# Performance work log

Measured on AMD Instinct MI355X. Metric: run time of the kernel, lower is better.

The kernel has to match this reference:

```python
import jax, jax.numpy as jnp
import numpy as np

N_AGENTS = 8; N_DUMMY = 16; BATCH = 1024; PLAN = 128; HID = 256

def setup_inputs():
    key = jax.random.key(0)
    ks = jax.random.split(key, 12)
    N, ND, B, P, H = N_AGENTS, N_DUMMY, BATCH, PLAN, HID
    plans = jax.random.normal(ks[0], (B, N, P), jnp.float32)
    keep = jax.random.bernoulli(ks[1], 0.7, (B, N))  # ragged communication pattern
    comm_plans = jax.random.normal(ks[2], (B, N, P), jnp.float32) * keep[:, :, None]
    coord_hiddens = 0.1 * jax.random.normal(ks[3], (N, 2, B, H), jnp.float32)
    dummy_noise = jax.random.normal(ks[4], (N, ND - N, B, 2 * P), jnp.float32)
    s = 0.05
    Wi_f = s * jax.random.normal(ks[5], (N, 3 * H, 2 * P), jnp.float32)
    Wh_f = s * jax.random.normal(ks[6], (N, 3 * H, H), jnp.float32)
    Wi_b = s * jax.random.normal(ks[7], (N, 3 * H, 2 * P), jnp.float32)
    Wh_b = s * jax.random.normal(ks[8], (N, 3 * H, H), jnp.float32)
    ln_g = jnp.ones((N, 2 * H), jnp.float32)
    ln_b = jnp.zeros((N, 2 * H), jnp.float32)
    W1 = s * jax.random.normal(ks[9], (N, H, 2 * H), jnp.float32)
    b1 = jnp.zeros((N, H), jnp.float32)
    W2 = s * jax.random.normal(ks[10], (N, 2, H), jnp.float32)
    b2 = jnp.zeros((N, 2), jnp.float32)
    return dict(plans=plans, comm_plans=comm_plans, coord_hiddens=coord_hiddens,
                dummy_noise=dummy_noise, Wi_f=Wi_f, Wh_f=Wh_f, Wi_b=Wi_b, Wh_b=Wh_b,
                ln_g=ln_g, ln_b=ln_b, W1=W1, b1=b1, W2=W2, b2=b2)

def _gru_scan(xs, h0, Wi, Wh, valid):
    # PyTorch GRU cell (biases are zero-initialized in RecurrentHead), length-masked
    H = h0.shape[-1]
    gi_all = jnp.einsum('tbi,gi->tbg', xs, Wi)  # (T,B,3H) input projections, one GEMM
    def step(h, inp):
        gi, v = inp
        gh = h @ Wh.T
        r = jax.nn.sigmoid(gi[:, :H] + gh[:, :H])
        z = jax.nn.sigmoid(gi[:, H:2 * H] + gh[:, H:2 * H])
        n = jnp.tanh(gi[:, 2 * H:] + r * gh[:, 2 * H:])
        hn = (1.0 - z) * n + z * h
        h = jnp.where(v[:, None], hn, h)            # packed: no update past seq end
        return h, jnp.where(v[:, None], hn, 0.0)    # pad_packed returns zeros there
    hT, out = jax.lax.scan(step, h0, (gi_all, valid))
    return out, hT

def _forward(plans, comm_plans, coord_hiddens, dummy_noise, Wi_f, Wh_f, Wi_b, Wh_b, ln_g, ln_b, W1, b1, W2, b2):
    B, N, P = plans.shape
    ND = N_DUMMY
    # comm_plans[~any(any(comm_plans))] = plans[...]
    empty = ~jnp.any(jnp.any(comm_plans != 0, -1), -1)            # (B,)
    comm = jnp.where(empty[:, None, None], plans, comm_plans)     # (B,N,P)
    mask_real = jnp.any(comm != 0, -1).T                          # (N,B)
    mask = jnp.concatenate([mask_real, jnp.ones((ND - N, B), bool)], 0)  # (ND,B)
    mask_flat = mask.reshape(-1)
    seq_len = mask.sum(0)                                         # (B,)
    t_idx = jnp.arange(ND)[:, None]
    packed_mask = t_idx < seq_len[None, :]                        # (ND,B)
    pm_flat = packed_mask.reshape(-1)
    # torch boolean-index / masked_scatter consume elements in flat row-major order;
    # we reproduce those exact semantics.
    src_idx = jnp.nonzero(mask_flat, size=ND * B, fill_value=0)[0]
    rank_pack = jnp.cumsum(pm_flat) - 1
    cum_scat = jnp.cumsum(mask_flat) - 1
    rev_idx = jnp.where(packed_mask, seq_len[None, :] - 1 - t_idx, 0)

    def pack(x):  # compact_seq[packed_mask] = x[batch_mask]
        xf = x.reshape(ND * B, -1)
        return jnp.where(pm_flat[:, None], xf[src_idx[rank_pack]], 0.0).reshape(ND, B, -1)

    def scatter(s):  # zeros.masked_scatter(mask, scores)
        st, sb = cum_scat // B, cum_scat % B
        return jnp.where(mask_flat[:, None], s[st, sb], 0.0).reshape(ND, B, -1)

    def rev(a):  # per-column reversal within valid length (for bidirectional GRU)
        g = jnp.take_along_axis(a, jnp.broadcast_to(rev_idx[:, :, None], a.shape), axis=0)
        return jnp.where(packed_mask[:, :, None], g, 0.0)

    plans_t = plans.transpose(1, 0, 2)  # (N,B,P): plans[:, i] per agent

    def per_agent(plan_i, dn_i, hxs_i, wif, whf, wib, whb, g, bta, w1, bb1, w2, bb2):
        others = jnp.concatenate([jnp.broadcast_to(plan_i[:, None, :], comm.shape), comm], -1)  # (B,N,2P)
        x = jnp.concatenate([others.transpose(1, 0, 2), dn_i], 0)  # (ND,B,2P) with randn dummy rows
        cseq = pack(x)
        out_f, hf = _gru_scan(cseq, hxs_i[0], wif, whf, packed_mask)
        out_b_r, hb = _gru_scan(rev(cseq), hxs_i[1], wib, whb, packed_mask)
        out_b = rev(out_b_r)
        scores = scatter(jnp.concatenate([out_f, out_b], -1))  # (ND,B,2H)
        mu = scores.mean(-1, keepdims=True)
        var = ((scores - mu) ** 2).mean(-1, keepdims=True)
        scores = (scores - mu) * jax.lax.rsqrt(var + 1e-5) * g + bta  # LayerNorm
        h1 = jax.nn.relu(jnp.einsum('tbc,hc->tbh', scores, w1) + bb1)
        cm = jnp.einsum('tbh,oh->tbo', h1, w2) + bb2               # (ND,B,2)
        return cm, jnp.stack([hf, hb])                              # (2,B,H)

    coord_masks, coord_rnn_hxs = jax.vmap(per_agent)(
        plans_t, dummy_noise, coord_hiddens, Wi_f, Wh_f, Wi_b, Wh_b, ln_g, ln_b, W1, b1, W2, b2)
    return coord_masks, coord_rnn_hxs

def reference(plans, comm_plans, coord_hiddens, dummy_noise, Wi_f, Wh_f, Wi_b, Wh_b, ln_g, ln_b, W1, b1, W2, b2):
    return _forward(plans, comm_plans, coord_hiddens, dummy_noise, Wi_f, Wh_f, Wi_b, Wh_b, ln_g, ln_b, W1, b1, W2, b2)
```

## Files before the change

### kernel.cpp

```cpp
#include <hip/hip_runtime.h>


typedef _Float16 f16;
typedef __attribute__((ext_vector_type(4))) _Float16 f16x4;
typedef __attribute__((ext_vector_type(8))) _Float16 f16x8;
typedef __attribute__((ext_vector_type(4))) float floatx4;

__device__ __forceinline__ float sigf(float x) { return 1.0f / (1.0f + __expf(-x)); }
__device__ __forceinline__ float tanhfast(float x) {
    float e = __expf(2.0f * x);
    return 1.0f - 2.0f / (e + 1.0f);
}

__device__ __forceinline__ void gl16(const f16* g, f16* l) {
    __builtin_amdgcn_global_load_lds((const __attribute__((address_space(1))) void*)g,
                                     (__attribute__((address_space(3))) void*)l,
                                     16, 0, 0);
}

__global__ void k_empty(const float* __restrict__ comm, int* __restrict__ empty) {
    int b = blockIdx.x;
    __shared__ int flag;
    if (threadIdx.x == 0) flag = 0;
    __syncthreads();
    const float* p = comm + (size_t)b * 1024;
    int any = 0;
    for (int e = threadIdx.x; e < 1024; e += 256)
        if (p[e] != 0.0f) any = 1;
    if (any) flag = 1;
    __syncthreads();
    if (threadIdx.x == 0) empty[b] = (flag == 0);
}

__global__ void k_mask(const float* __restrict__ plans, const float* __restrict__ comm,
                       const int* __restrict__ empty, int* __restrict__ mask) {
    int row = blockIdx.x * 4 + (threadIdx.x >> 6);
    int lane = threadIdx.x & 63;
    int t = row >> 10, b = row & 1023;
    int m;
    if (t >= 8) {
        m = 1;
    } else {
        const float* src = (empty[b] ? plans : comm) + ((size_t)b * 8 + t) * 128;
        float v0 = src[lane * 2], v1 = src[lane * 2 + 1];
        m = __any((v0 != 0.0f) || (v1 != 0.0f)) ? 1 : 0;
    }
    if (lane == 0) mask[row] = m;
}

__global__ void k_scan(const int* __restrict__ mask, int* __restrict__ seq_len,
                       int* __restrict__ pack_src, int* __restrict__ scat_src,
                       int* __restrict__ inv_scat) {
    __shared__ int s_sl[1024];
    __shared__ int s_m[1024];
    __shared__ int s_p[1024];
    __shared__ unsigned short s_idx[16384];
    int tid = threadIdx.x;
    int sl = 8;
    for (int t = 0; t < 8; t++) sl += mask[t * 1024 + tid];
    s_sl[tid] = sl;
    seq_len[tid] = sl;
    __syncthreads();
    int mv[16], pv[16];
    int mc = 0, pc = 0;
    int j0 = tid * 16;
    for (int q = 0; q < 16; q++) {
        int j = j0 + q;
        mv[q] = mask[j];
        pv[q] = ((j >> 10) < s_sl[j & 1023]) ? 1 : 0;
        mc += mv[q]; pc += pv[q];
    }
    s_m[tid] = mc; s_p[tid] = pc;
    __syncthreads();
    for (int off = 1; off < 1024; off <<= 1) {
        int am = (tid >= off) ? s_m[tid - off] : 0;
        int ap = (tid >= off) ? s_p[tid - off] : 0;
        __syncthreads();
        s_m[tid] += am; s_p[tid] += ap;
        __syncthreads();
    }
    if (tid == 1023) seq_len[1024] = s_m[1023];
    int moff = s_m[tid] - mc;
    int poff = s_p[tid] - pc;
    int rm = moff;
    for (int q = 0; q < 16; q++)
        if (mv[q]) s_idx[rm++] = (unsigned short)(j0 + q);
    __syncthreads();
    rm = moff;
    int rp = poff;
    for (int q = 0; q < 16; q++) {
        int j = j0 + q;
        scat_src[j] = mv[q] ? rm : -1;
        if (mv[q]) { inv_scat[rm] = j; rm++; }
        pack_src[j] = pv[q] ? (int)s_idx[rp] : -1;
        if (pv[q]) rp++;
    }
}

__global__ void k_pack(const float* __restrict__ plans, const float* __restrict__ comm,
                       const float* __restrict__ dummy, const int* __restrict__ empty,
                       const int* __restrict__ pack_src, f16* __restrict__ cseq) {
    int row = blockIdx.x * 8 + (threadIdx.x >> 5);
    int lane = threadIdx.x & 31;
    int i = row >> 14;
    int j = row & 16383;
    int s = pack_src[j];
    f16x8 o = {0, 0, 0, 0, 0, 0, 0, 0};
    if (s >= 0) {
        int tp = s >> 10, bp = s & 1023;
        const float* src;
        if (tp < 8) {
            if (lane < 16) src = plans + ((size_t)bp * 8 + i) * 128 + lane * 8;
            else src = (empty[bp] ? plans : comm) + ((size_t)bp * 8 + tp) * 128 + (lane - 16) * 8;
        } else {
            src = dummy + (((size_t)i * 8 + (tp - 8)) * 1024 + bp) * 256 + lane * 8;
        }
        float4 v0 = *(const float4*)src;
        float4 v1 = *(const float4*)(src + 4);
        o[0] = (f16)v0.x; o[1] = (f16)v0.y; o[2] = (f16)v0.z; o[3] = (f16)v0.w;
        o[4] = (f16)v1.x; o[5] = (f16)v1.y; o[6] = (f16)v1.z; o[7] = (f16)v1.w;
    }
    *(f16x8*)(cseq + ((size_t)row << 8) + lane * 8) = o;
}

__global__ void k_prep_w(const float* __restrict__ Wi_f, const float* __restrict__ Wh_f,
                         const float* __restrict__ Wi_b, const float* __restrict__ Wh_b,
                         f16* __restrict__ whalf) {
    int ch2 = blockIdx.y;
    int ch = ch2 >> 1, sel = ch2 & 1;
    int i = ch >> 1, d = ch & 1;
    const float* src = sel ? (d ? Wh_b : Wh_f) : (d ? Wi_b : Wi_f);
    src += (size_t)i * 196608;
    int off = (blockIdx.x * 256 + threadIdx.x) * 4;
    float4 v = *(const float4*)(src + off);
    f16x4 o = { (f16)v.x, (f16)v.y, (f16)v.z, (f16)v.w };
    *(f16x4*)(whalf + (size_t)ch2 * 196608 + off) = o;
}

__global__ void k_prep_w1(const float* __restrict__ W1, f16* __restrict__ w1half) {
    int off = (blockIdx.x * 256 + threadIdx.x) * 4;
    float4 v = *(const float4*)(W1 + off);
    f16x4 o = { (f16)v.x, (f16)v.y, (f16)v.z, (f16)v.w };
    *(f16x4*)(w1half + off) = o;
}

__global__ void k_init_h(const float* __restrict__ hx, float* __restrict__ h,
                         f16* __restrict__ hh0) {
    int e = (blockIdx.x * 256 + threadIdx.x) * 4;
    float4 v = *(const float4*)(hx + e);
    *(float4*)(h + e) = v;
    f16x4 o = { (f16)v.x, (f16)v.y, (f16)v.z, (f16)v.w };
    *(f16x4*)(hh0 + e) = o;
}

__global__ void k_zfill(const int* __restrict__ scat_src, const int* __restrict__ seq_len,
                        f16* __restrict__ scores) {
    int j = blockIdx.x;
    int tid = threadIdx.x;
    int c = scat_src[j];
    if (c < 0) {
        for (int i = 0; i < 8; i++) {
            unsigned int* p = (unsigned int*)(scores + ((size_t)(i * 16384 + j)) * 512);
            p[tid] = 0u;
        }
    } else {
        int st = c >> 10, sb = c & 1023;
        if (st >= seq_len[sb] && tid < 128) {
            for (int i = 0; i < 8; i++) {
                unsigned int* p = (unsigned int*)(scores + ((size_t)(i * 16384 + j)) * 512 + 256);
                p[tid] = 0u;
            }
        }
    }
}

__global__ __launch_bounds__(256, 2) void k_step(
    const f16* __restrict__ cseq, const f16* __restrict__ whalf,
    float* __restrict__ h, const f16* __restrict__ hh_in, f16* __restrict__ hh_out,
    f16* __restrict__ scores, const int* __restrict__ seq_len,
    const int* __restrict__ inv_scat, int t)
{
    __shared__ f16 lA[128 * 64];
    __shared__ f16 lB[192 * 64];
    int bx = blockIdx.x;
    int ch = bx & 15;
    int mt = (bx >> 4) & 7;
    int nt = bx >> 7;
    int i = ch >> 1, d = ch & 1;
    int tid = threadIdx.x;
    int lane = tid & 63, w = tid >> 6;
    int li = lane & 15, q = lane >> 4;
    int rsub = lane >> 3;
    int sc = (lane & 7) ^ rsub;

    const f16* pA[4]; const f16* pH[4]; const f16* pB[6];
#pragma unroll
    for (int p = 0; p < 4; p++) {
        int ar = (w * 4 + p) * 8 + rsub;
        int b = mt * 128 + ar;
        int tt = t;
        if (d) { int sl = seq_len[b]; tt = sl - 1 - t; if (tt < 0) tt = 0; }
        pA[p] = cseq + (((size_t)i * 16 + tt) * 1024 + b) * 256 + sc * 8;
        pH[p] = hh_in + ((size_t)ch * 1024 + b) * 256 + sc * 8;
    }
#pragma unroll
    for (int p = 0; p < 6; p++) {
        int nr = (w * 6 + p) * 8 + rsub;
        int g = (nr >> 6) * 256 + nt * 64 + (nr & 63);
        pB[p] = whalf + (size_t)(ch * 2) * 196608 + (size_t)g * 256 + sc * 8;
    }

    floatx4 accr[4][2], accz[4][2], accgi[4][2], accgh[4][2];
    floatx4 z4 = {0.f, 0.f, 0.f, 0.f};
#pragma unroll
    for (int n = 0; n < 4; n++)
        for (int s = 0; s < 2; s++) { accr[n][s] = z4; accz[n][s] = z4; accgi[n][s] = z4; accgh[n][s] = z4; }

    for (int kt = 0; kt < 512; kt += 64) {
        bool xph = (kt < 256);
        if (xph) {
#pragma unroll
            for (int p = 0; p < 4; p++) gl16(pA[p] + kt, &lA[(w * 4 + p) * 512]);
#pragma unroll
            for (int p = 0; p < 6; p++) gl16(pB[p] + kt, &lB[(w * 6 + p) * 512]);
        } else {
#pragma unroll
            for (int p = 0; p < 4; p++) gl16(pH[p] + (kt - 256), &lA[(w * 4 + p) * 512]);
#pragma unroll
            for (int p = 0; p < 6; p++) gl16(pB[p] + 196608 + (kt - 256), &lB[(w * 6 + p) * 512]);
        }
        __syncthreads();
#pragma unroll
        for (int kk = 0; kk < 64; kk += 32) {
            int sw = ((q + (kk >> 3)) ^ (li & 7)) << 3;
            f16x8 a0 = *(f16x8*)&lA[(w * 32 + li) * 64 + sw];
            f16x8 a1 = *(f16x8*)&lA[(w * 32 + 16 + li) * 64 + sw];
#pragma unroll
            for (int n = 0; n < 4; n++) {
                f16x8 br = *(f16x8*)&lB[(n * 16 + li) * 64 + sw];
                f16x8 bz = *(f16x8*)&lB[(64 + n * 16 + li) * 64 + sw];
                f16x8 bn = *(f16x8*)&lB[(128 + n * 16 + li) * 64 + sw];
                accr[n][0] = __builtin_amdgcn_mfma_f32_16x16x32_f16(a0, br, accr[n][0], 0, 0, 0);
                accr[n][1] = __builtin_amdgcn_mfma_f32_16x16x32_f16(a1, br, accr[n][1], 0, 0, 0);
                accz[n][0] = __builtin_amdgcn_mfma_f32_16x16x32_f16(a0, bz, accz[n][0], 0, 0, 0);
                accz[n][1] = __builtin_amdgcn_mfma_f32_16x16x32_f16(a1, bz, accz[n][1], 0, 0, 0);
                if (xph) {
                    accgi[n][0] = __builtin_amdgcn_mfma_f32_16x16x32_f16(a0, bn, accgi[n][0], 0, 0, 0);
                    accgi[n][1] = __builtin_amdgcn_mfma_f32_16x16x32_f16(a1, bn, accgi[n][1], 0, 0, 0);
                } else {
                    accgh[n][0] = __builtin_amdgcn_mfma_f32_16x16x32_f16(a0, bn, accgh[n][0], 0, 0, 0);
                    accgh[n][1] = __builtin_amdgcn_mfma_f32_16x16x32_f16(a1, bn, accgh[n][1], 0, 0, 0);
                }
            }
        }
        __syncthreads();
    }

    int T = seq_len[1024];
#pragma unroll
    for (int s = 0; s < 2; s++) {
#pragma unroll
        for (int r = 0; r < 4; r++) {
            int b = mt * 128 + w * 32 + s * 16 + q * 4 + r;
            int sl = seq_len[b];
            int v = (t < sl);
            int st = d ? (sl - 1 - t) : t;
            int cfl = st * 1024 + b;
            int j = -1;
            if (d == 0) { if (cfl < T) j = inv_scat[cfl]; }
            else        { if (v && cfl < T) j = inv_scat[cfl]; }
#pragma unroll
            for (int n = 0; n < 4; n++) {
                int c = nt * 64 + n * 16 + li;
                float rg = sigf(accr[n][s][r]);
                float zg = sigf(accz[n][s][r]);
                float nn = tanhfast(accgi[n][s][r] + rg * accgh[n][s][r]);
                size_t hidx = ((size_t)ch * 1024 + b) * 256 + c;
                float hp = h[hidx];
                float hn = (1.0f - zg) * nn + zg * hp;
                float hnew = v ? hn : hp;
                h[hidx] = hnew;
                hh_out[hidx] = (f16)hnew;
                if (j >= 0)
                    scores[((size_t)(i * 16384 + j)) * 512 + d * 256 + c] = (f16)(v ? hn : 0.0f);
            }
        }
    }
}

__global__ __launch_bounds__(512, 4) void k_mlp(
    const f16* __restrict__ scores,
    const float* __restrict__ ln_g, const float* __restrict__ ln_b,
    const f16* __restrict__ w1half, const float* __restrict__ b1,
    const float* __restrict__ W2, const float* __restrict__ b2,
    float* __restrict__ out)
{
    __shared__ f16 lA[128 * 64];
    __shared__ f16 lB[256 * 64];
    __shared__ float s_mu[128], s_rs[128];
    int bx = blockIdx.x;
    int i = bx >> 7, mt = bx & 127;
    int tid = threadIdx.x, lane = tid & 63, w = tid >> 6, li = lane & 15, q = lane >> 4;
    int rsub = lane >> 3;
    int sc = (lane & 7) ^ rsub;

    {
        int r = tid >> 2, sub = tid & 3;
        const f16* sp = scores + ((size_t)(i * 16384 + mt * 128 + r)) * 512 + sub * 128;
        float s = 0.f, sq = 0.f;
#pragma unroll
        for (int e = 0; e < 16; e++) {
            uint4 raw = *(const uint4*)(sp + e * 8);
            f16x8 v = *(f16x8*)&raw;
#pragma unroll
            for (int u = 0; u < 8; u++) { float f = (float)v[u]; s += f; sq += f * f; }
        }
        s += __shfl_xor(s, 1); sq += __shfl_xor(sq, 1);
        s += __shfl_xor(s, 2); sq += __shfl_xor(sq, 2);
        if (sub == 0) {
            float mu = s * (1.0f / 512.0f);
            float var = sq * (1.0f / 512.0f) - mu * mu;
            if (var < 0.f) var = 0.f;
            s_mu[r] = mu;
            s_rs[r] = rsqrtf(var + 1e-5f);
        }
    }

    const f16* pB[4];
#pragma unroll
    for (int p = 0; p < 4; p++) {
        int nr = (w * 4 + p) * 8 + rsub;
        pB[p] = w1half + ((size_t)i * 256 + nr) * 512 + sc * 8;
    }

    floatx4 acc[16];
    floatx4 z4 = {0.f, 0.f, 0.f, 0.f};
#pragma unroll
    for (int n = 0; n < 16; n++) acc[n] = z4;
    __syncthreads();

    for (int kt = 0; kt < 512; kt += 64) {
#pragma unroll
        for (int p = 0; p < 2; p++) {
            int e = p * 512 + tid;
            int ar = e >> 3, chk = e & 7;
            int m = mt * 128 + ar;
            uint4 raw = *(const uint4*)(scores + ((size_t)(i * 16384 + m)) * 512 + kt + chk * 8);
            f16x8 sv = *(f16x8*)&raw;
            float mu = s_mu[ar], rs = s_rs[ar];
            int co = i * 512 + kt + chk * 8;
            float4 g0 = *(const float4*)(ln_g + co);
            float4 g1 = *(const float4*)(ln_g + co + 4);
            float4 t0 = *(const float4*)(ln_b + co);
            float4 t1 = *(const float4*)(ln_b + co + 4);
            f16x8 ov;
            ov[0] = (f16)(((float)sv[0] - mu) * rs * g0.x + t0.x);
            ov[1] = (f16)(((float)sv[1] - mu) * rs * g0.y + t0.y);
            ov[2] = (f16)(((float)sv[2] - mu) * rs * g0.z + t0.z);
            ov[3] = (f16)(((float)sv[3] - mu) * rs * g0.w + t0.w);
            ov[4] = (f16)(((float)sv[4] - mu) * rs * g1.x + t1.x);
            ov[5] = (f16)(((float)sv[5] - mu) * rs * g1.y + t1.y);
            ov[6] = (f16)(((float)sv[6] - mu) * rs * g1.z + t1.z);
            ov[7] = (f16)(((float)sv[7] - mu) * rs * g1.w + t1.w);
            *(f16x8*)&lA[ar * 64 + ((chk ^ (ar & 7)) << 3)] = ov;
        }
#pragma unroll
        for (int p = 0; p < 4; p++) gl16(pB[p] + kt, &lB[(w * 4 + p) * 512]);
        __syncthreads();
#pragma unroll
        for (int kk = 0; kk < 64; kk += 32) {
            int sw = ((q + (kk >> 3)) ^ (li & 7)) << 3;
            f16x8 a = *(f16x8*)&lA[(w * 16 + li) * 64 + sw];
#pragma unroll
            for (int n = 0; n < 16; n++) {
                f16x8 bb = *(f16x8*)&lB[(n * 16 + li) * 64 + sw];
                acc[n] = __builtin_amdgcn_mfma_f32_16x16x32_f16(a, bb, acc[n], 0, 0, 0);
            }
        }
        __syncthreads();
    }

    float b1v[16], w2a[16], w2b[16];
#pragma unroll
    for (int n = 0; n < 16; n++) {
        int col = n * 16 + li;
        b1v[n] = b1[i * 256 + col];
        w2a[n] = W2[((size_t)i * 2 + 0) * 256 + col];
        w2b[n] = W2[((size_t)i * 2 + 1) * 256 + col];
    }
    float b2a = b2[i * 2], b2b = b2[i * 2 + 1];
#pragma unroll
    for (int r = 0; r < 4; r++) {
        float p0 = 0.f, p1 = 0.f;
#pragma unroll
        for (int n = 0; n < 16; n++) {
            float h1 = acc[n][r] + b1v[n];
            h1 = fmaxf(h1, 0.0f);
            p0 += h1 * w2a[n];
            p1 += h1 * w2b[n];
        }
#pragma unroll
        for (int off = 1; off < 16; off <<= 1) { p0 += __shfl_xor(p0, off); p1 += __shfl_xor(p1, off); }
        if (li == 0) {
            int m = mt * 128 + w * 16 + q * 4 + r;
            size_t oi = ((size_t)i * 16384 + m) * 2;
            out[oi]     = p0 + b2a;
            out[oi + 1] = p1 + b2b;
        }
    }
}

__global__ void k_hout(const float* __restrict__ h, float* __restrict__ out) {
    int e = (blockIdx.x * 256 + threadIdx.x) * 4;
    *(float4*)(out + 262144 + e) = *(const float4*)(h + e);
}

extern "C" void kernel_launch(void* const* d_in, const int* in_sizes, int n_in,
                              void* d_out, int out_size, void* d_ws, size_t ws_size,
                              hipStream_t stream)
{
    const float* plans = (const float*)d_in[0];
    const float* comm  = (const float*)d_in[1];
    const float* hx    = (const float*)d_in[2];
    const float* dummy = (const float*)d_in[3];
    const float* Wi_f  = (const float*)d_in[4];
    const float* Wh_f  = (const float*)d_in[5];
    const float* Wi_b  = (const float*)d_in[6];
    const float* Wh_b  = (const float*)d_in[7];
    const float* ln_g  = (const float*)d_in[8];
    const float* ln_b  = (const float*)d_in[9];
    const float* W1    = (const float*)d_in[10];
    const float* b1    = (const float*)d_in[11];
    const float* W2    = (const float*)d_in[12];
    const float* b2    = (const float*)d_in[13];
    float* out = (float*)d_out;

    char* ws = (char*)d_ws;
    f16*    cseq    = (f16*)   (ws + 0);
    f16*    scores  = (f16*)   (ws + 67108864);
    float*  h       = (float*) (ws + 201326592);
    f16*    hh0     = (f16*)   (ws + 218103808);
    f16*    hh1     = (f16*)   (ws + 226492416);
    f16*    whalf   = (f16*)   (ws + 234881024);
    f16*    w1half  = (f16*)   (ws + 247463936);
    int*    empty   = (int*)   (ws + 250609664);
    int*    seq_len = (int*)   (ws + 250613760);
    int*    maskb   = (int*)   (ws + 250621952);
    int*    pack_s  = (int*)   (ws + 250687488);
    int*    scat_s  = (int*)   (ws + 250753024);
    int*    inv_s   = (int*)   (ws + 250818560);
    if (ws_size < 250884096ULL) return;

    k_empty<<<1024, 256, 0, stream>>>(comm, empty);
    k_mask<<<4096, 256, 0, stream>>>(plans, comm, empty, maskb);
    k_scan<<<1, 1024, 0, stream>>>(maskb, seq_len, pack_s, scat_s, inv_s);
    k_pack<<<16384, 256, 0, stream>>>(plans, comm, dummy, empty, pack_s, cseq);
    k_zfill<<<16384, 256, 0, stream>>>(scat_s, seq_len, scores);
    k_prep_w<<<dim3(192, 32), 256, 0, stream>>>(Wi_f, Wh_f, Wi_b, Wh_b, whalf);
    k_prep_w1<<<1024, 256, 0, stream>>>(W1, w1half);
    k_init_h<<<4096, 256, 0, stream>>>(hx, h, hh0);
    for (int t = 0; t < 16; t++) {
        f16* hin  = (t & 1) ? hh1 : hh0;
        f16* hout = (t & 1) ? hh0 : hh1;
        k_step<<<512, 256, 0, stream>>>(cseq, whalf, h, hin, hout, scores,
                                        seq_len, inv_s, t);
    }
    k_mlp<<<1024, 512, 0, stream>>>(scores, ln_g, ln_b, w1half, b1, W2, b2, out);
    k_hout<<<4096, 256, 0, stream>>>(h, out);
}
```

Baseline: 738.0 us.

## Fuse per-timestep GRU launches into one persistent kernel with register-resident hidden state

Replaces the 16 per-timestep k_step launches, plus the separate h-init and h-output kernels, with one k_gru kernel. Each block owns 64 batch rows of one agent/direction chain for all 256 hidden units across every timestep. The hidden state stays in registers, with an f16 copy in LDS for the recurrent GEMM. The next step's input rows are prefetched into LDS while the gate nonlinearities run. This removes launch overhead and the global round-trips of h between steps. In exchange, each block now streams the full input and recurrent weight matrices from global/L2 straight into registers every step. Only 256 blocks run, so occupancy is low.

Result: slower. 1.492 ms (+102.2%).

```diff
diff --git a/kernel.cpp b/kernel.cpp
--- a/kernel.cpp
+++ b/kernel.cpp
@@ -144,15 +144,6 @@
     *(f16x4*)(w1half + off) = o;
 }
 
-__global__ void k_init_h(const float* __restrict__ hx, float* __restrict__ h,
-                         f16* __restrict__ hh0) {
-    int e = (blockIdx.x * 256 + threadIdx.x) * 4;
-    float4 v = *(const float4*)(hx + e);
-    *(float4*)(h + e) = v;
-    f16x4 o = { (f16)v.x, (f16)v.y, (f16)v.z, (f16)v.w };
-    *(f16x4*)(hh0 + e) = o;
-}
-
 __global__ void k_zfill(const int* __restrict__ scat_src, const int* __restrict__ seq_len,
                         f16* __restrict__ scores) {
     int j = blockIdx.x;
@@ -174,117 +165,178 @@
     }
 }
 
-__global__ __launch_bounds__(256, 2) void k_step(
+__global__ __launch_bounds__(512, 2) void k_gru(
     const f16* __restrict__ cseq, const f16* __restrict__ whalf,
-    float* __restrict__ h, const f16* __restrict__ hh_in, f16* __restrict__ hh_out,
-    f16* __restrict__ scores, const int* __restrict__ seq_len,
-    const int* __restrict__ inv_scat, int t)
+    const float* __restrict__ hx, f16* __restrict__ scores,
+    const int* __restrict__ seq_len, const int* __restrict__ inv_scat,
+    float* __restrict__ out)
 {
-    __shared__ f16 lA[128 * 64];
-    __shared__ f16 lB[192 * 64];
-    int bx = blockIdx.x;
-    int ch = bx & 15;
-    int mt = (bx >> 4) & 7;
-    int nt = bx >> 7;
-    int i = ch >> 1, d = ch & 1;
-    int tid = threadIdx.x;
-    int lane = tid & 63, w = tid >> 6;
-    int li = lane & 15, q = lane >> 4;
-    int rsub = lane >> 3;
-    int sc = (lane & 7) ^ rsub;
-
-    const f16* pA[4]; const f16* pH[4]; const f16* pB[6];
+    __shared__ f16 lX[64 * 256];
+    __shared__ f16 lH[64 * 256];
+    const int bx = blockIdx.x;
+    const int ch = bx & 15;
+    const int mt = bx >> 4;
+    const int i = ch >> 1, d = ch & 1;
+    const int tid = threadIdx.x;
+    const int lane = tid & 63, w = tid >> 6;
+    const int li = lane & 15, q = lane >> 4;
+    const int x7 = li & 7;
+
+    int bst[4], scp[4], slst[4];
+    {
+        int sub2 = lane >> 5;
+        int ss = lane & 31;
+        int sg = ss >> 3, sb = ss & 7;
+#pragma unroll
+        for (int p = 0; p < 4; p++) {
+            int r8 = 2 * p + sub2;
+            bst[p] = mt * 64 + w * 8 + r8;
+            scp[p] = (sg * 8 + (sb ^ r8)) * 8;
+            slst[p] = seq_len[bst[p]];
+        }
+    }
+    const int T = seq_len[1024];
+
+    int slmr[4][4];
+    float hreg[4][2][4];
+#pragma unroll
+    for (int m = 0; m < 4; m++)
+#pragma unroll
+        for (int r = 0; r < 4; r++) {
+            int b = mt * 64 + m * 16 + q * 4 + r;
+            slmr[m][r] = seq_len[b];
+            int row = m * 16 + q * 4 + r;
+#pragma unroll
+            for (int n = 0; n < 2; n++) {
+                int c = w * 32 + n * 16 + li;
+                float v = hx[((size_t)ch * 1024 + b) * 256 + c];
+                hreg[m][n][r] = v;
+                lH[row * 256 + (c >> 6) * 64 + ((((c >> 3) & 7) ^ (row & 7)) << 3) + (c & 7)] = (f16)v;
+            }
+        }
+
+    const f16* wb = whalf + (size_t)(ch * 2) * 196608 + (size_t)li * 256 + q * 8;
+    int O[3][2];
+#pragma unroll
+    for (int g = 0; g < 3; g++)
+#pragma unroll
+        for (int n = 0; n < 2; n++)
+            O[g][n] = (g * 256 + w * 32 + n * 16) * 256;
+
 #pragma unroll
     for (int p = 0; p < 4; p++) {
-        int ar = (w * 4 + p) * 8 + rsub;
-        int b = mt * 128 + ar;
-        int tt = t;
-        if (d) { int sl = seq_len[b]; tt = sl - 1 - t; if (tt < 0) tt = 0; }
-        pA[p] = cseq + (((size_t)i * 16 + tt) * 1024 + b) * 256 + sc * 8;
-        pH[p] = hh_in + ((size_t)ch * 1024 + b) * 256 + sc * 8;
-    }
-#pragma unroll
-    for (int p = 0; p < 6; p++) {
-        int nr = (w * 6 + p) * 8 + rsub;
-        int g = (nr >> 6) * 256 + nt * 64 + (nr & 63);
-        pB[p] = whalf + (size_t)(ch * 2) * 196608 + (size_t)g * 256 + sc * 8;
+        int tt = d ? (slst[p] - 1) : 0;
+        gl16(cseq + (((size_t)i * 16 + tt) * 1024 + bst[p]) * 256 + scp[p],
+             &lX[(w * 8 + 2 * p) * 256]);
     }
 
     floatx4 accr[4][2], accz[4][2], accgi[4][2], accgh[4][2];
-    floatx4 z4 = {0.f, 0.f, 0.f, 0.f};
-#pragma unroll
-    for (int n = 0; n < 4; n++)
-        for (int s = 0; s < 2; s++) { accr[n][s] = z4; accz[n][s] = z4; accgi[n][s] = z4; accgh[n][s] = z4; }
-
-    for (int kt = 0; kt < 512; kt += 64) {
-        bool xph = (kt < 256);
-        if (xph) {
-#pragma unroll
-            for (int p = 0; p < 4; p++) gl16(pA[p] + kt, &lA[(w * 4 + p) * 512]);
-#pragma unroll
-            for (int p = 0; p < 6; p++) gl16(pB[p] + kt, &lB[(w * 6 + p) * 512]);
-        } else {
-#pragma unroll
-            for (int p = 0; p < 4; p++) gl16(pH[p] + (kt - 256), &lA[(w * 4 + p) * 512]);
-#pragma unroll
-            for (int p = 0; p < 6; p++) gl16(pB[p] + 196608 + (kt - 256), &lB[(w * 6 + p) * 512]);
-        }
+    const floatx4 z4 = {0.f, 0.f, 0.f, 0.f};
+
+#pragma unroll 1
+    for (int t = 0; t < 16; t++) {
+#pragma unroll
+        for (int m = 0; m < 4; m++)
+#pragma unroll
+            for (int n = 0; n < 2; n++) {
+                accr[m][n] = z4; accz[m][n] = z4; accgi[m][n] = z4; accgh[m][n] = z4;
+            }
         __syncthreads();
-#pragma unroll
-        for (int kk = 0; kk < 64; kk += 32) {
-            int sw = ((q + (kk >> 3)) ^ (li & 7)) << 3;
-            f16x8 a0 = *(f16x8*)&lA[(w * 32 + li) * 64 + sw];
-            f16x8 a1 = *(f16x8*)&lA[(w * 32 + 16 + li) * 64 + sw];
-#pragma unroll
-            for (int n = 0; n < 4; n++) {
-                f16x8 br = *(f16x8*)&lB[(n * 16 + li) * 64 + sw];
-                f16x8 bz = *(f16x8*)&lB[(64 + n * 16 + li) * 64 + sw];
-                f16x8 bn = *(f16x8*)&lB[(128 + n * 16 + li) * 64 + sw];
-                accr[n][0] = __builtin_amdgcn_mfma_f32_16x16x32_f16(a0, br, accr[n][0], 0, 0, 0);
-                accr[n][1] = __builtin_amdgcn_mfma_f32_16x16x32_f16(a1, br, accr[n][1], 0, 0, 0);
-                accz[n][0] = __builtin_amdgcn_mfma_f32_16x16x32_f16(a0, bz, accz[n][0], 0, 0, 0);
-                accz[n][1] = __builtin_amdgcn_mfma_f32_16x16x32_f16(a1, bz, accz[n][1], 0, 0, 0);
-                if (xph) {
-                    accgi[n][0] = __builtin_amdgcn_mfma_f32_16x16x32_f16(a0, bn, accgi[n][0], 0, 0, 0);
-                    accgi[n][1] = __builtin_amdgcn_mfma_f32_16x16x32_f16(a1, bn, accgi[n][1], 0, 0, 0);
-                } else {
-                    accgh[n][0] = __builtin_amdgcn_mfma_f32_16x16x32_f16(a0, bn, accgh[n][0], 0, 0, 0);
-                    accgh[n][1] = __builtin_amdgcn_mfma_f32_16x16x32_f16(a1, bn, accgh[n][1], 0, 0, 0);
+
+#pragma unroll
+        for (int kk = 0; kk < 8; kk++) {
+            int sw = (kk >> 1) * 64 + ((((kk & 1) * 4 + q) ^ x7) << 3);
+            f16x8 a0 = *(const f16x8*)&lX[(0 * 16 + li) * 256 + sw];
+            f16x8 a1 = *(const f16x8*)&lX[(1 * 16 + li) * 256 + sw];
+            f16x8 a2 = *(const f16x8*)&lX[(2 * 16 + li) * 256 + sw];
+            f16x8 a3 = *(const f16x8*)&lX[(3 * 16 + li) * 256 + sw];
+#pragma unroll
+            for (int n = 0; n < 2; n++) {
+                f16x8 br = *(const f16x8*)(wb + O[0][n] + kk * 32);
+                f16x8 bz = *(const f16x8*)(wb + O[1][n] + kk * 32);
+                f16x8 bn = *(const f16x8*)(wb + O[2][n] + kk * 32);
+                accr[0][n] = __builtin_amdgcn_mfma_f32_16x16x32_f16(a0, br, accr[0][n], 0, 0, 0);
+                accr[1][n] = __builtin_amdgcn_mfma_f32_16x16x32_f16(a1, br, accr[1][n], 0, 0, 0);
+                accr[2][n] = __builtin_amdgcn_mfma_f32_16x16x32_f16(a2, br, accr[2][n], 0, 0, 0);
+                accr[3][n] = __builtin_amdgcn_mfma_f32_16x16x32_f16(a3, br, accr[3][n], 0, 0, 0);
+                accz[0][n] = __builtin_amdgcn_mfma_f32_16x16x32_f16(a0, bz, accz[0][n], 0, 0, 0);
+                accz[1][n] = __builtin_amdgcn_mfma_f32_16x16x32_f16(a1, bz, accz[1][n], 0, 0, 0);
+                accz[2][n] = __builtin_amdgcn_mfma_f32_16x16x32_f16(a2, bz, accz[2][n], 0, 0, 0);
+                accz[3][n] = __builtin_amdgcn_mfma_f32_16x16x32_f16(a3, bz, accz[3][n], 0, 0, 0);
+                accgi[0][n] = __builtin_amdgcn_mfma_f32_16x16x32_f16(a0, bn, accgi[0][n], 0, 0, 0);
+                accgi[1][n] = __builtin_amdgcn_mfma_f32_16x16x32_f16(a1, bn, accgi[1][n], 0, 0, 0);
+                accgi[2][n] = __builtin_amdgcn_mfma_f32_16x16x32_f16(a2, bn, accgi[2][n], 0, 0, 0);
+                accgi[3][n] = __builtin_amdgcn_mfma_f32_16x16x32_f16(a3, bn, accgi[3][n], 0, 0, 0);
+            }
+        }
+#pragma unroll
+        for (int kk = 0; kk < 8; kk++) {
+            int sw = (kk >> 1) * 64 + ((((kk & 1) * 4 + q) ^ x7) << 3);
+            f16x8 a0 = *(const f16x8*)&lH[(0 * 16 + li) * 256 + sw];
+            f16x8 a1 = *(const f16x8*)&lH[(1 * 16 + li) * 256 + sw];
+            f16x8 a2 = *(const f16x8*)&lH[(2 * 16 + li) * 256 + sw];
+            f16x8 a3 = *(const f16x8*)&lH[(3 * 16 + li) * 256 + sw];
+#pragma unroll
+            for (int n = 0; n < 2; n++) {
+                f16x8 br = *(const f16x8*)(wb + 196608 + O[0][n] + kk * 32);
+                f16x8 bz = *(const f16x8*)(wb + 196608 + O[1][n] + kk * 32);
+                f16x8 bn = *(const f16x8*)(wb + 196608 + O[2][n] + kk * 32);
+                accr[0][n] = __builtin_amdgcn_mfma_f32_16x16x32_f16(a0, br, accr[0][n], 0, 0, 0);
+                accr[1][n] = __builtin_amdgcn_mfma_f32_16x16x32_f16(a1, br, accr[1][n], 0, 0, 0);
+                accr[2][n] = __builtin_amdgcn_mfma_f32_16x16x32_f16(a2, br, accr[2][n], 0, 0, 0);
+                accr[3][n] = __builtin_amdgcn_mfma_f32_16x16x32_f16(a3, br, accr[3][n], 0, 0, 0);
+                accz[0][n] = __builtin_amdgcn_mfma_f32_16x16x32_f16(a0, bz, accz[0][n], 0, 0, 0);
+                accz[1][n] = __builtin_amdgcn_mfma_f32_16x16x32_f16(a1, bz, accz[1][n], 0, 0, 0);
+                accz[2][n] = __builtin_amdgcn_mfma_f32_16x16x32_f16(a2, bz, accz[2][n], 0, 0, 0);
+                accz[3][n] = __builtin_amdgcn_mfma_f32_16x16x32_f16(a3, bz, accz[3][n], 0, 0, 0);
+                accgh[0][n] = __builtin_amdgcn_mfma_f32_16x16x32_f16(a0, bn, accgh[0][n], 0, 0, 0);
+                accgh[1][n] = __builtin_amdgcn_mfma_f32_16x16x32_f16(a1, bn, accgh[1][n], 0, 0, 0);
+                accgh[2][n] = __builtin_amdgcn_mfma_f32_16x16x32_f16(a2, bn, accgh[2][n], 0, 0, 0);
+                accgh[3][n] = __builtin_amdgcn_mfma_f32_16x16x32_f16(a3, bn, accgh[3][n], 0, 0, 0);
+            }
+        }
+        __syncthreads();
+
+        if (t < 15) {
+#pragma unroll
+            for (int p = 0; p < 4; p++) {
+                int tt = t + 1;
+                if (d) { tt = slst[p] - 2 - t; if (tt < 0) tt = 0; }
+                gl16(cseq + (((size_t)i * 16 + tt) * 1024 + bst[p]) * 256 + scp[p],
+                     &lX[(w * 8 + 2 * p) * 256]);
+            }
+        }
+
+#pragma unroll
+        for (int m = 0; m < 4; m++)
+#pragma unroll
+            for (int r = 0; r < 4; r++) {
+                int b = mt * 64 + m * 16 + q * 4 + r;
+                int sl = slmr[m][r];
+                int v = (t < sl);
+                int st = d ? (sl - 1 - t) : t;
+                int cfl = st * 1024 + b;
+                int j = -1;
+                if (d == 0) { if (cfl < T) j = inv_scat[cfl]; }
+                else        { if (v && cfl < T) j = inv_scat[cfl]; }
+                int row = m * 16 + q * 4 + r;
+#pragma unroll
+                for (int n = 0; n < 2; n++) {
+                    int c = w * 32 + n * 16 + li;
+                    float rg = sigf(accr[m][n][r]);
+                    float zg = sigf(accz[m][n][r]);
+                    float nn = tanhfast(accgi[m][n][r] + rg * accgh[m][n][r]);
+                    float hp = hreg[m][n][r];
+                    float hn = (1.0f - zg) * nn + zg * hp;
+                    float hnew = v ? hn : hp;
+                    hreg[m][n][r] = hnew;
+                    lH[row * 256 + (c >> 6) * 64 + ((((c >> 3) & 7) ^ (row & 7)) << 3) + (c & 7)] = (f16)hnew;
+                    if (j >= 0)
+                        scores[((size_t)(i * 16384 + j)) * 512 + d * 256 + c] = (f16)(v ? hn : 0.0f);
+                    if (t == 15)
+                        out[262144 + ((size_t)ch * 1024 + b) * 256 + c] = hnew;
                 }
             }
-        }
-        __syncthreads();
-    }
-
-    int T = seq_len[1024];
-#pragma unroll
-    for (int s = 0; s < 2; s++) {
-#pragma unroll
-        for (int r = 0; r < 4; r++) {
-            int b = mt * 128 + w * 32 + s * 16 + q * 4 + r;
-            int sl = seq_len[b];
-            int v = (t < sl);
-            int st = d ? (sl - 1 - t) : t;
-            int cfl = st * 1024 + b;
-            int j = -1;
-            if (d == 0) { if (cfl < T) j = inv_scat[cfl]; }
-            else        { if (v && cfl < T) j = inv_scat[cfl]; }
-#pragma unroll
-            for (int n = 0; n < 4; n++) {
-                int c = nt * 64 + n * 16 + li;
-                float rg = sigf(accr[n][s][r]);
-                float zg = sigf(accz[n][s][r]);
-                float nn = tanhfast(accgi[n][s][r] + rg * accgh[n][s][r]);
-                size_t hidx = ((size_t)ch * 1024 + b) * 256 + c;
-                float hp = h[hidx];
-                float hn = (1.0f - zg) * nn + zg * hp;
-                float hnew = v ? hn : hp;
-                h[hidx] = hnew;
-                hh_out[hidx] = (f16)hnew;
-                if (j >= 0)
-                    scores[((size_t)(i * 16384 + j)) * 512 + d * 256 + c] = (f16)(v ? hn : 0.0f);
-            }
-        }
     }
 }
 
@@ -410,11 +462,6 @@
     }
 }
 
-__global__ void k_hout(const float* __restrict__ h, float* __restrict__ out) {
-    int e = (blockIdx.x * 256 + threadIdx.x) * 4;
-    *(float4*)(out + 262144 + e) = *(const float4*)(h + e);
-}
-
 extern "C" void kernel_launch(void* const* d_in, const int* in_sizes, int n_in,
                               void* d_out, int out_size, void* d_ws, size_t ws_size,
                               hipStream_t stream)
@@ -438,9 +485,6 @@
     char* ws = (char*)d_ws;
     f16*    cseq    = (f16*)   (ws + 0);
     f16*    scores  = (f16*)   (ws + 67108864);
-    float*  h       = (float*) (ws + 201326592);
-    f16*    hh0     = (f16*)   (ws + 218103808);
-    f16*    hh1     = (f16*)   (ws + 226492416);
     f16*    whalf   = (f16*)   (ws + 234881024);
     f16*    w1half  = (f16*)   (ws + 247463936);
     int*    empty   = (int*)   (ws + 250609664);
@@ -458,13 +502,6 @@
     k_zfill<<<16384, 256, 0, stream>>>(scat_s, seq_len, scores);
     k_prep_w<<<dim3(192, 32), 256, 0, stream>>>(Wi_f, Wh_f, Wi_b, Wh_b, whalf);
     k_prep_w1<<<1024, 256, 0, stream>>>(W1, w1half);
-    k_init_h<<<4096, 256, 0, stream>>>(hx, h, hh0);
-    for (int t = 0; t < 16; t++) {
-        f16* hin  = (t & 1) ? hh1 : hh0;
-        f16* hout = (t & 1) ? hh0 : hh1;
-        k_step<<<512, 256, 0, stream>>>(cseq, whalf, h, hin, hout, scores,
-                                        seq_len, inv_s, t);
-    }
+    k_gru<<<256, 512, 0, stream>>>(cseq, whalf, hx, scores, seq_len, inv_s, out);
     k_mlp<<<1024, 512, 0, stream>>>(scores, ln_g, ln_b, w1half, b1, W2, b2, out);
-    k_hout<<<4096, 256, 0, stream>>>(h, out);
-}
+}
```
